# Optimization experiments

Measured on AMD Instinct MI355X. Metric: run time of the kernel, lower is better.

Reference implementation:

```python
import jax, jax.numpy as jnp
import numpy as np

B, C, H, W = 2, 256, 80, 160
G, P, E = 8, 8, 2  # groups(heads), sampling points, ffn expansion
LN_EPS = 1e-5


def setup_inputs() -> dict:
    key = jax.random.key(0)
    ks = jax.random.split(key, 12)
    def n(k, shape, s=1.0):
        return jax.random.normal(k, shape, dtype=jnp.float32) * s
    return dict(
        feats=n(ks[0], (B, C, H, W)),
        feats_pos=n(ks[1], (B, C, H, W)),
        anchor_points=jax.random.uniform(ks[2], (B, H, W, 2), dtype=jnp.float32),
        value_W=n(ks[3], (C, C), 0.02), value_b=jnp.zeros((C,), jnp.float32),
        off_W=n(ks[4], (C, G * P * 2), 0.02), off_b=n(ks[5], (G * P * 2,), 0.02),
        attn_W=n(ks[6], (C, G * P), 0.02), attn_b=jnp.zeros((G * P,), jnp.float32),
        out_W=n(ks[7], (C, C), 0.02), out_b=jnp.zeros((C,), jnp.float32),
        ln1_g=jnp.ones((C,), jnp.float32), ln1_b=jnp.zeros((C,), jnp.float32),
        ln2_g=jnp.ones((C,), jnp.float32), ln2_b=jnp.zeros((C,), jnp.float32),
        ffn_w1=n(ks[8], (E * C, C), 0.02), ffn_b1=jnp.zeros((E * C,), jnp.float32),
        ffn_w2=n(ks[9], (C, E * C), 0.02), ffn_b2=jnp.zeros((C,), jnp.float32),
    )


def _layernorm(x, g, b):
    m = jnp.mean(x, axis=-1, keepdims=True)
    v = jnp.mean(jnp.square(x - m), axis=-1, keepdims=True)
    return (x - m) * jax.lax.rsqrt(v + LN_EPS) * g + b


def _bilinear_sample(value, px, py, h, w):
    # value: [b,G,HW,cg]; px,py: [b,G,P,HW] pixel coords (align_corners=False)
    x0 = jnp.floor(px); y0 = jnp.floor(py)
    wx1 = px - x0; wx0 = 1.0 - wx1
    wy1 = py - y0; wy0 = 1.0 - wy1
    vexp = value[:, :, None, :, :]  # [b,G,1,HW,cg]
    def gather(xi, yi):
        valid = ((xi >= 0) & (xi < w) & (yi >= 0) & (yi < h)).astype(value.dtype)
        xc = jnp.clip(xi, 0, w - 1).astype(jnp.int32)
        yc = jnp.clip(yi, 0, h - 1).astype(jnp.int32)
        idx = yc * w + xc  # [b,G,P,HW]
        v = jnp.take_along_axis(vexp, idx[..., None], axis=3)  # [b,G,P,HW,cg]
        return v * valid[..., None]
    return (gather(x0, y0) * (wx0 * wy0)[..., None]
            + gather(x0 + 1, y0) * (wx1 * wy0)[..., None]
            + gather(x0, y0 + 1) * (wx0 * wy1)[..., None]
            + gather(x0 + 1, y0 + 1) * (wx1 * wy1)[..., None])


def reference(feats, feats_pos, anchor_points,
              value_W, value_b, off_W, off_b, attn_W, attn_b, out_W, out_b,
              ln1_g, ln1_b, ln2_g, ln2_b, ffn_w1, ffn_b1, ffn_w2, ffn_b2):
    b, c, h, w = feats.shape
    hw = h * w
    cg = c // G
    x = feats + feats_pos                              # residual input (pos-encoded)
    q = x.reshape(b, c, hw).transpose(0, 2, 1)         # [b,HW,c]
    # deformable attention
    val = (q @ value_W + value_b).reshape(b, hw, G, cg).transpose(0, 2, 1, 3)   # [b,G,HW,cg]
    off = (q @ off_W + off_b).reshape(b, hw, G, P, 2).transpose(0, 2, 3, 1, 4)  # [b,G,P,HW,2]
    attn = jax.nn.softmax((q @ attn_W + attn_b).reshape(b, hw, G, P)
                          .transpose(0, 2, 3, 1), axis=2)                        # [b,G,P,HW]
    anchor = anchor_points.reshape(b, hw, 2)[:, None, None, :, :]               # [b,1,1,HW,2]
    loc = anchor + off / jnp.array([w, h], dtype=off.dtype)                     # normalized xy
    px = loc[..., 0] * w - 0.5
    py = loc[..., 1] * h - 0.5
    sampled = _bilinear_sample(val, px, py, h, w)                               # [b,G,P,HW,cg]
    agg = jnp.einsum('bgpn,bgpnc->bngc', attn, sampled).reshape(b, hw, c)
    upd = agg @ out_W + out_b
    # residual + LN1
    y = _layernorm(q + upd, ln1_g, ln1_b)
    # conv1x1 - SiLU - conv1x1 FFN + residual + LN2
    ffn = jax.nn.silu(y @ ffn_w1.T + ffn_b1) @ ffn_w2.T + ffn_b2
    y = _layernorm(y + ffn, ln2_g, ln2_b)
    return y.transpose(0, 2, 1).reshape(b, c, h, w)
```

## Files before the change

### kernel.cpp

```cpp
#include <hip/hip_runtime.h>
#include <hip/hip_bf16.h>
#include <math.h>
#include <stdint.h>

#define B_ 2
#define C_ 256
#define H_ 80
#define W_ 160
#define HW_ (H_*W_)
#define NTOK (B_*HW_)
#define G_ 8
#define P_ 8
#define NQKV 448
#define NQKVP 512

typedef __bf16 bf16;
typedef __attribute__((ext_vector_type(8))) __bf16 bf16x8;
typedef __attribute__((ext_vector_type(4))) float f32x4;

__device__ __forceinline__ void gload_lds16(const void* g, void* l) {
  __builtin_amdgcn_global_load_lds(
      (__attribute__((address_space(1))) void*)g,
      (__attribute__((address_space(3))) void*)l,
      16, 0, 0);
}

__global__ __launch_bounds__(256)
void prep_weights(const float* __restrict__ vW, const float* __restrict__ vb,
                  const float* __restrict__ oW, const float* __restrict__ ob,
                  const float* __restrict__ aW, const float* __restrict__ ab,
                  const float* __restrict__ outW,
                  const float* __restrict__ w1, const float* __restrict__ w2,
                  bf16* __restrict__ wqkv, float* __restrict__ bqkv,
                  bf16* __restrict__ woutt, bf16* __restrict__ w1b, bf16* __restrict__ w2b)
{
  int i = blockIdx.x * 256 + threadIdx.x;
  if (i < NQKVP*256) {
    int nn = i >> 8, k = i & 255;
    float w;
    if (nn < 256)      w = vW[k*256 + nn];
    else if (nn < 384) w = oW[k*128 + (nn-256)];
    else if (nn < 448) w = aW[k*64  + (nn-384)];
    else               w = 0.f;
    wqkv[i] = (bf16)w;
  }
  int j = i - NQKVP*256;
  if (j >= 0 && j < 256*256) {
    int nn = j >> 8, k = j & 255;
    woutt[j] = (bf16)outW[k*256 + nn];
  }
  int j2 = i - (NQKVP*256 + 256*256);
  if (j2 >= 0 && j2 < 512*256) w1b[j2] = (bf16)w1[j2];
  int j3 = i - (NQKVP*256 + 256*256 + 512*256);
  if (j3 >= 0 && j3 < 256*512) w2b[j3] = (bf16)w2[j3];
  int j4 = i - (NQKVP*256 + 256*256 + 512*256 + 256*512);
  if (j4 >= 0 && j4 < NQKVP) {
    float bv;
    if (j4 < 256)      bv = vb[j4];
    else if (j4 < 384) bv = ob[j4-256];
    else if (j4 < 448) bv = ab[j4-384];
    else               bv = 0.f;
    bqkv[j4] = bv;
  }
}

__global__ __launch_bounds__(256)
void qprep_kernel(const float* __restrict__ f, const float* __restrict__ fp,
                  bf16* __restrict__ qb)
{
  __shared__ float lt[64][65];
  const int tid = threadIdx.x;
  const int n0 = blockIdx.x * 64;
  const int c0 = blockIdx.y * 64;
  const int b  = blockIdx.z;
#pragma unroll
  for (int i = 0; i < 16; ++i) {
    int cl = i*4 + (tid >> 6), nl = tid & 63;
    size_t gi = ((size_t)(b*C_ + c0 + cl))*HW_ + n0 + nl;
    lt[cl][nl] = f[gi] + fp[gi];
  }
  __syncthreads();
#pragma unroll
  for (int i = 0; i < 16; ++i) {
    int nl = i*4 + (tid >> 6), cl = tid & 63;
    size_t qi = ((size_t)(b*HW_ + n0 + nl))*C_ + c0 + cl;
    qb[qi] = (bf16)lt[cl][nl];
  }
}

template<int EPI, int KTOT>
__global__ __launch_bounds__(256)
void gemm_kernel(const bf16* __restrict__ A, const bf16* __restrict__ Bt,
                 const float* __restrict__ bias,
                 void* __restrict__ out0, float* __restrict__ out1,
                 float* __restrict__ out2, const bf16* __restrict__ resb)
{
  __shared__ bf16 lA[128*64];
  __shared__ bf16 lB[128*64];
  const int tid  = threadIdx.x;
  const int wave = tid >> 6, lane = tid & 63;
  const int m0 = blockIdx.x * 128, n0 = blockIdx.y * 128;
  const int wm = wave >> 1, wn = wave & 1;
  const int fr = lane & 15;
  const int fq = lane >> 4;
  f32x4 acc[4][4] = {};

  for (int kc = 0; kc < KTOT/64; ++kc) {
    if (kc) __syncthreads();
#pragma unroll
    for (int it = 0; it < 4; ++it) {
      int chunk = it*256 + tid;
      int row = chunk >> 3, cb = chunk & 7;
      int ksw = ((cb ^ (row & 7)) << 3);
      gload_lds16(A  + (size_t)(m0+row)*KTOT + kc*64 + ksw,
                  (char*)lA + it*4096 + wave*1024);
      gload_lds16(Bt + (size_t)(n0+row)*KTOT + kc*64 + ksw,
                  (char*)lB + it*4096 + wave*1024);
    }
    __syncthreads();
#pragma unroll
    for (int ks = 0; ks < 2; ++ks) {
      bf16x8 af[4], bg[4];
#pragma unroll
      for (int i = 0; i < 4; ++i) {
        int ar = wm*64 + i*16 + fr;
        af[i] = *(const bf16x8*)&lA[ar*64 + (((ks*4 + fq) ^ (ar & 7)) << 3)];
        int br = wn*64 + i*16 + fr;
        bg[i] = *(const bf16x8*)&lB[br*64 + (((ks*4 + fq) ^ (br & 7)) << 3)];
      }
#pragma unroll
      for (int mi = 0; mi < 4; ++mi)
#pragma unroll
        for (int ni = 0; ni < 4; ++ni)
          acc[mi][ni] = __builtin_amdgcn_mfma_f32_16x16x32_bf16(af[mi], bg[ni], acc[mi][ni], 0, 0, 0);
    }
  }

#pragma unroll
  for (int mi = 0; mi < 4; ++mi)
#pragma unroll
  for (int ni = 0; ni < 4; ++ni)
#pragma unroll
  for (int r = 0; r < 4; ++r) {
    int row = m0 + wm*64 + mi*16 + fq*4 + r;
    int col = n0 + wn*64 + ni*16 + fr;
    float v = acc[mi][ni][r] + bias[col];
    if (EPI == 0) {
      if (col < 256)      ((bf16*)out0)[(size_t)row*256 + col] = (bf16)v;
      else if (col < 384) out1[(size_t)row*128 + (col-256)] = v;
      else if (col < 448) out2[(size_t)row*64  + (col-384)] = v;
    } else if (EPI == 2) {
      float s = v / (1.0f + __expf(-v));
      ((bf16*)out0)[(size_t)row*512 + col] = (bf16)s;
    } else {
      ((float*)out0)[(size_t)row*256 + col] = v + (float)resb[(size_t)row*256 + col];
    }
  }
}

__global__ __launch_bounds__(512)
void gemm_ln_kernel(const bf16* __restrict__ A, const bf16* __restrict__ Bt,
                    const float* __restrict__ bias, const bf16* __restrict__ res,
                    const float* __restrict__ gg, const float* __restrict__ bb,
                    bf16* __restrict__ y1b)
{
  __shared__ bf16 lA[128*64];
  __shared__ bf16 lB[256*64];
  __shared__ float2 red[128][4];
  const int tid  = threadIdx.x;
  const int wave = tid >> 6, lane = tid & 63;
  const int m0 = blockIdx.x * 128;
  const int wm = wave >> 2, wn = wave & 3;
  const int fr = lane & 15;
  const int fq = lane >> 4;
  f32x4 acc[4][4] = {};

  for (int kc = 0; kc < 256/64; ++kc) {
    if (kc) __syncthreads();
#pragma unroll
    for (int it = 0; it < 2; ++it) {
      int chunk = it*512 + tid;
      int row = chunk >> 3, cb = chunk & 7;
      int ksw = ((cb ^ (row & 7)) << 3);
      gload_lds16(A + (size_t)(m0+row)*256 + kc*64 + ksw,
                  (char*)lA + it*8192 + wave*1024);
    }
#pragma unroll
    for (int it = 0; it < 4; ++it) {
      int chunk = it*512 + tid;
      int row = chunk >> 3, cb = chunk & 7;
      int ksw = ((cb ^ (row & 7)) << 3);
      gload_lds16(Bt + (size_t)row*256 + kc*64 + ksw,
                  (char*)lB + it*8192 + wave*1024);
    }
    __syncthreads();
#pragma unroll
    for (int ks = 0; ks < 2; ++ks) {
      bf16x8 af[4], bg[4];
#pragma unroll
      for (int i = 0; i < 4; ++i) {
        int ar = wm*64 + i*16 + fr;
        af[i] = *(const bf16x8*)&lA[ar*64 + (((ks*4 + fq) ^ (ar & 7)) << 3)];
        int br = wn*64 + i*16 + fr;
        bg[i] = *(const bf16x8*)&lB[br*64 + (((ks*4 + fq) ^ (br & 7)) << 3)];
      }
#pragma unroll
      for (int mi = 0; mi < 4; ++mi)
#pragma unroll
        for (int ni = 0; ni < 4; ++ni)
          acc[mi][ni] = __builtin_amdgcn_mfma_f32_16x16x32_bf16(af[mi], bg[ni], acc[mi][ni], 0, 0, 0);
    }
  }

  float gcol[4], bcol[4];
#pragma unroll
  for (int ni = 0; ni < 4; ++ni) {
    int col = wn*64 + ni*16 + fr;
    gcol[ni] = gg[col]; bcol[ni] = bb[col];
  }
#pragma unroll
  for (int mi = 0; mi < 4; ++mi)
#pragma unroll
  for (int r = 0; r < 4; ++r) {
    int rowl = wm*64 + mi*16 + fq*4 + r;
    size_t rowg = (size_t)(m0 + rowl);
    float s = 0.f, q = 0.f;
#pragma unroll
    for (int ni = 0; ni < 4; ++ni) {
      int col = wn*64 + ni*16 + fr;
      float v = acc[mi][ni][r] + bias[col] + (float)res[rowg*256 + col];
      acc[mi][ni][r] = v;
      s += v; q += v*v;
    }
#pragma unroll
    for (int o = 1; o < 16; o <<= 1) { s += __shfl_xor(s, o, 64); q += __shfl_xor(q, o, 64); }
    if (fr == 0) red[rowl][wn] = make_float2(s, q);
  }
  __syncthreads();
#pragma unroll
  for (int mi = 0; mi < 4; ++mi)
#pragma unroll
  for (int r = 0; r < 4; ++r) {
    int rowl = wm*64 + mi*16 + fq*4 + r;
    size_t rowg = (size_t)(m0 + rowl);
    float s = 0.f, q = 0.f;
#pragma unroll
    for (int k = 0; k < 4; ++k) { float2 p = red[rowl][k]; s += p.x; q += p.y; }
    const float mean = s * (1.f/256.f);
    const float var  = q * (1.f/256.f) - mean*mean;
    const float rs   = rsqrtf(var + 1e-5f);
#pragma unroll
    for (int ni = 0; ni < 4; ++ni) {
      int col = wn*64 + ni*16 + fr;
      float y = (acc[mi][ni][r] - mean)*rs*gcol[ni] + bcol[ni];
      y1b[rowg*256 + col] = (bf16)y;
    }
  }
}

__global__ __launch_bounds__(256)
void sample_kernel(const bf16* __restrict__ val, const float* __restrict__ off,
                   const float* __restrict__ attnl, const float* __restrict__ anchors,
                   bf16* __restrict__ agg)
{
  const int tid  = threadIdx.x;
  const int lane = tid & 63;
  const int wv   = tid >> 6;
  const int tsub = lane >> 5;
  const int g    = (lane >> 2) & 7;
  const int c8   = lane & 3;
  const int t    = blockIdx.x * 8 + wv * 2 + tsub;
  const int b    = t / HW_;

  const float2 anc = *(const float2*)(anchors + (size_t)t*2);
  const float ax = anc.x * W_ - 0.5f;
  const float ay = anc.y * H_ - 0.5f;

  const float4 l0 = *(const float4*)(attnl + (size_t)t*64 + g*8);
  const float4 l1 = *(const float4*)(attnl + (size_t)t*64 + g*8 + 4);
  float l[8] = {l0.x, l0.y, l0.z, l0.w, l1.x, l1.y, l1.z, l1.w};
  float mx = l[0];
#pragma unroll
  for (int p = 1; p < 8; ++p) mx = fmaxf(mx, l[p]);
  float s = 0.f;
#pragma unroll
  for (int p = 0; p < 8; ++p) { l[p] = __expf(l[p] - mx); s += l[p]; }
  const float inv = 1.f / s;

  const float4* opv = (const float4*)(off + (size_t)t*128 + g*16);
  const float4 o0 = opv[0], o1 = opv[1], o2 = opv[2], o3 = opv[3];
  const float ox[8] = {o0.x, o0.z, o1.x, o1.z, o2.x, o2.z, o3.x, o3.z};
  const float oy[8] = {o0.y, o0.w, o1.y, o1.w, o2.y, o2.w, o3.y, o3.w};

  const bf16* vb = val + ((size_t)b*HW_)*256 + g*32 + c8*8;

  float a[8] = {};
#pragma unroll
  for (int p = 0; p < 8; ++p) {
    const float px = ax + ox[p], py = ay + oy[p];
    const float x0f = floorf(px), y0f = floorf(py);
    const int x0 = (int)x0f, y0 = (int)y0f;
    const float wx1 = px - x0f, wx0 = 1.f - wx1;
    const float wy1 = py - y0f, wy0 = 1.f - wy1;
    const float ap = l[p] * inv;
    float w00 = ap*wx0*wy0, w10 = ap*wx1*wy0, w01 = ap*wx0*wy1, w11 = ap*wx1*wy1;
    const bool vx0 = (unsigned)x0 < W_, vx1 = (unsigned)(x0+1) < W_;
    const bool vy0 = (unsigned)y0 < H_, vy1 = (unsigned)(y0+1) < H_;
    w00 = (vx0 && vy0) ? w00 : 0.f;  w10 = (vx1 && vy0) ? w10 : 0.f;
    w01 = (vx0 && vy1) ? w01 : 0.f;  w11 = (vx1 && vy1) ? w11 : 0.f;
    const int xc0 = min(max(x0, 0), W_-1),   xc1 = min(max(x0+1, 0), W_-1);
    const int yc0 = min(max(y0, 0), H_-1),   yc1 = min(max(y0+1, 0), H_-1);
    const bf16x8 v00 = *(const bf16x8*)(vb + (size_t)(yc0*W_ + xc0)*256);
    const bf16x8 v10 = *(const bf16x8*)(vb + (size_t)(yc0*W_ + xc1)*256);
    const bf16x8 v01 = *(const bf16x8*)(vb + (size_t)(yc1*W_ + xc0)*256);
    const bf16x8 v11 = *(const bf16x8*)(vb + (size_t)(yc1*W_ + xc1)*256);
#pragma unroll
    for (int c = 0; c < 8; ++c)
      a[c] += w00*(float)v00[c] + w10*(float)v10[c]
            + w01*(float)v01[c] + w11*(float)v11[c];
  }
  bf16 r[8];
#pragma unroll
  for (int c = 0; c < 8; ++c) r[c] = (bf16)a[c];
  *(bf16x8*)(agg + (size_t)t*256 + g*32 + c8*8) = *(bf16x8*)r;
}

__global__ __launch_bounds__(256)
void ln2_out_kernel(const float* __restrict__ x, const float* __restrict__ gg,
                    const float* __restrict__ bb, float* __restrict__ out)
{
  __shared__ float lt[32][257];
  const int tid = threadIdx.x, wave = tid >> 6, lane = tid & 63;
  const int tok0 = blockIdx.x * 32;
#pragma unroll
  for (int t8 = 0; t8 < 8; ++t8) {
    const int tl = wave*8 + t8;
    const size_t tok = tok0 + tl;
    const float4 v = ((const float4*)(x + tok*256))[lane];
    float s = v.x + v.y + v.z + v.w;
    float q = v.x*v.x + v.y*v.y + v.z*v.z + v.w*v.w;
#pragma unroll
    for (int o = 32; o; o >>= 1) { s += __shfl_xor(s, o, 64); q += __shfl_xor(q, o, 64); }
    const float mean = s * (1.f/256.f);
    const float var  = q * (1.f/256.f) - mean*mean;
    const float rs   = rsqrtf(var + 1e-5f);
    const int c = lane*4;
    lt[tl][c+0] = (v.x - mean)*rs*gg[c+0] + bb[c+0];
    lt[tl][c+1] = (v.y - mean)*rs*gg[c+1] + bb[c+1];
    lt[tl][c+2] = (v.z - mean)*rs*gg[c+2] + bb[c+2];
    lt[tl][c+3] = (v.w - mean)*rs*gg[c+3] + bb[c+3];
  }
  __syncthreads();
  const int b  = tok0 / HW_;
  const int n0 = tok0 % HW_;
#pragma unroll
  for (int it = 0; it < 32; ++it) {
    int flat = it*256 + tid;
    int c = flat >> 5, tl = flat & 31;
    out[((size_t)(b*C_ + c))*HW_ + n0 + tl] = lt[tl][c];
  }
}

extern "C" void kernel_launch(void* const* d_in, const int* in_sizes, int n_in,
                              void* d_out, int out_size, void* d_ws, size_t ws_size,
                              hipStream_t stream)
{
  const float* feats   = (const float*)d_in[0];
  const float* featsp  = (const float*)d_in[1];
  const float* anchors = (const float*)d_in[2];
  const float* value_W = (const float*)d_in[3];
  const float* value_b = (const float*)d_in[4];
  const float* off_W   = (const float*)d_in[5];
  const float* off_b   = (const float*)d_in[6];
  const float* attn_W  = (const float*)d_in[7];
  const float* attn_b  = (const float*)d_in[8];
  const float* out_W   = (const float*)d_in[9];
  const float* out_b   = (const float*)d_in[10];
  const float* ln1_g   = (const float*)d_in[11];
  const float* ln1_b   = (const float*)d_in[12];
  const float* ln2_g   = (const float*)d_in[13];
  const float* ln2_b   = (const float*)d_in[14];
  const float* w1      = (const float*)d_in[15];
  const float* b1      = (const float*)d_in[16];
  const float* w2      = (const float*)d_in[17];
  const float* b2      = (const float*)d_in[18];
  float* out = (float*)d_out;

  char* ws = (char*)d_ws;
  size_t cur = 0;
  auto alloc = [&](size_t bytes) -> char* {
    char* p = ws + cur;
    cur += (bytes + 255) & ~(size_t)255;
    return p;
  };
  bf16*  wqkv  = (bf16*) alloc((size_t)NQKVP*256*2);
  bf16*  woutt = (bf16*) alloc((size_t)256*256*2);
  bf16*  w1b   = (bf16*) alloc((size_t)512*256*2);
  bf16*  w2b   = (bf16*) alloc((size_t)256*512*2);
  float* bqkv  = (float*)alloc((size_t)NQKVP*4);
  bf16*  qb    = (bf16*) alloc((size_t)NTOK*256*2);
  bf16*  valb  = (bf16*) alloc((size_t)NTOK*256*2);
  float* offv  = (float*)alloc((size_t)NTOK*128*4);
  float* attnl = (float*)alloc((size_t)NTOK*64*4);
  bf16*  aggb  = (bf16*) alloc((size_t)NTOK*256*2);
  bf16*  y1b   = (bf16*) alloc((size_t)NTOK*256*2);
  bf16*  hb    = (bf16*) alloc((size_t)NTOK*512*2);
  float* x2    = (float*)alloc((size_t)NTOK*256*4);

  prep_weights<<<(NQKVP*256 + 256*256 + 512*256 + 256*512 + NQKVP + 255)/256, 256, 0, stream>>>(
      value_W, value_b, off_W, off_b, attn_W, attn_b, out_W, w1, w2,
      wqkv, bqkv, woutt, w1b, w2b);

  qprep_kernel<<<dim3(HW_/64, C_/64, B_), 256, 0, stream>>>(feats, featsp, qb);

  gemm_kernel<0, 256><<<dim3(NTOK/128, NQKVP/128), 256, 0, stream>>>(
      qb, wqkv, bqkv, valb, offv, attnl, nullptr);

  sample_kernel<<<NTOK/8, 256, 0, stream>>>(valb, offv, attnl, anchors, aggb);

  gemm_ln_kernel<<<NTOK/128, 512, 0, stream>>>(
      aggb, woutt, out_b, qb, ln1_g, ln1_b, y1b);

  gemm_kernel<2, 256><<<dim3(NTOK/128, 512/128), 256, 0, stream>>>(
      y1b, w1b, b1, hb, nullptr, nullptr, nullptr);

  gemm_kernel<3, 512><<<dim3(NTOK/128, 256/128), 256, 0, stream>>>(
      hb, w2b, b2, x2, nullptr, nullptr, y1b);

  ln2_out_kernel<<<NTOK/32, 256, 0, stream>>>(x2, ln2_g, ln2_b, out);
}
```

Measured before the change: 152.9 us.

## Fuse FFN second GEMM with LayerNorm2 and NCHW transpose output

Replaces the FFN down-projection GEMM plus its separate LN2/transpose kernel with the templated gemm_ln_kernel. That kernel now handles KTOT=512, applies LayerNorm in registers, and writes NCHW float output through an LDS transpose that reuses the GEMM shared memory. This removes the fp32 x2 round trip through global memory and one launch. It also swizzles block indices in sample_kernel to spread tokens across blocks, aiming for better cache and channel locality. The fused kernel gains extra syncs and LDS transposes, and the full-row LN forces N=256 per block, which reduces grid parallelism.

```diff
diff --git a/kernel.cpp b/kernel.cpp
--- a/kernel.cpp
+++ b/kernel.cpp
@@ -93,7 +93,7 @@
 void gemm_kernel(const bf16* __restrict__ A, const bf16* __restrict__ Bt,
                  const float* __restrict__ bias,
                  void* __restrict__ out0, float* __restrict__ out1,
-                 float* __restrict__ out2, const bf16* __restrict__ resb)
+                 float* __restrict__ out2)
 {
   __shared__ bf16 lA[128*64];
   __shared__ bf16 lB[128*64];
@@ -149,23 +149,24 @@
       if (col < 256)      ((bf16*)out0)[(size_t)row*256 + col] = (bf16)v;
       else if (col < 384) out1[(size_t)row*128 + (col-256)] = v;
       else if (col < 448) out2[(size_t)row*64  + (col-384)] = v;
-    } else if (EPI == 2) {
+    } else {
       float s = v / (1.0f + __expf(-v));
       ((bf16*)out0)[(size_t)row*512 + col] = (bf16)s;
-    } else {
-      ((float*)out0)[(size_t)row*256 + col] = v + (float)resb[(size_t)row*256 + col];
-    }
-  }
-}
-
+    }
+  }
+}
+
+template<int KTOT, bool NCHW_OUT>
 __global__ __launch_bounds__(512)
 void gemm_ln_kernel(const bf16* __restrict__ A, const bf16* __restrict__ Bt,
                     const float* __restrict__ bias, const bf16* __restrict__ res,
                     const float* __restrict__ gg, const float* __restrict__ bb,
-                    bf16* __restrict__ y1b)
-{
-  __shared__ bf16 lA[128*64];
-  __shared__ bf16 lB[256*64];
+                    bf16* __restrict__ yb, float* __restrict__ outf)
+{
+  __shared__ __align__(16) char smem[49152];
+  bf16* lA = (bf16*)smem;
+  bf16* lB = (bf16*)(smem + 16384);
+  float (*lt)[132] = (float(*)[132])smem;
   __shared__ float2 red[128][4];
   const int tid  = threadIdx.x;
   const int wave = tid >> 6, lane = tid & 63;
@@ -175,14 +176,14 @@
   const int fq = lane >> 4;
   f32x4 acc[4][4] = {};
 
-  for (int kc = 0; kc < 256/64; ++kc) {
+  for (int kc = 0; kc < KTOT/64; ++kc) {
     if (kc) __syncthreads();
 #pragma unroll
     for (int it = 0; it < 2; ++it) {
       int chunk = it*512 + tid;
       int row = chunk >> 3, cb = chunk & 7;
       int ksw = ((cb ^ (row & 7)) << 3);
-      gload_lds16(A + (size_t)(m0+row)*256 + kc*64 + ksw,
+      gload_lds16(A + (size_t)(m0+row)*KTOT + kc*64 + ksw,
                   (char*)lA + it*8192 + wave*1024);
     }
 #pragma unroll
@@ -190,7 +191,7 @@
       int chunk = it*512 + tid;
       int row = chunk >> 3, cb = chunk & 7;
       int ksw = ((cb ^ (row & 7)) << 3);
-      gload_lds16(Bt + (size_t)row*256 + kc*64 + ksw,
+      gload_lds16(Bt + (size_t)row*KTOT + kc*64 + ksw,
                   (char*)lB + it*8192 + wave*1024);
     }
     __syncthreads();
@@ -242,7 +243,6 @@
 #pragma unroll
   for (int r = 0; r < 4; ++r) {
     int rowl = wm*64 + mi*16 + fq*4 + r;
-    size_t rowg = (size_t)(m0 + rowl);
     float s = 0.f, q = 0.f;
 #pragma unroll
     for (int k = 0; k < 4; ++k) { float2 p = red[rowl][k]; s += p.x; q += p.y; }
@@ -250,10 +250,45 @@
     const float var  = q * (1.f/256.f) - mean*mean;
     const float rs   = rsqrtf(var + 1e-5f);
 #pragma unroll
-    for (int ni = 0; ni < 4; ++ni) {
+    for (int ni = 0; ni < 4; ++ni)
+      acc[mi][ni][r] = (acc[mi][ni][r] - mean)*rs*gcol[ni] + bcol[ni];
+  }
+
+  if constexpr (!NCHW_OUT) {
+#pragma unroll
+    for (int mi = 0; mi < 4; ++mi)
+#pragma unroll
+    for (int ni = 0; ni < 4; ++ni)
+#pragma unroll
+    for (int r = 0; r < 4; ++r) {
+      size_t rowg = (size_t)(m0 + wm*64 + mi*16 + fq*4 + r);
       int col = wn*64 + ni*16 + fr;
-      float y = (acc[mi][ni][r] - mean)*rs*gcol[ni] + bcol[ni];
-      y1b[rowg*256 + col] = (bf16)y;
+      yb[rowg*256 + col] = (bf16)acc[mi][ni][r];
+    }
+  } else {
+    const int bq = m0 / HW_;
+    const int n0 = m0 % HW_;
+    __syncthreads();
+#pragma unroll
+    for (int ch = 0; ch < 4; ++ch) {
+      if (ch) __syncthreads();
+      if (wn == ch) {
+#pragma unroll
+        for (int mi = 0; mi < 4; ++mi)
+#pragma unroll
+        for (int ni = 0; ni < 4; ++ni)
+#pragma unroll
+        for (int r = 0; r < 4; ++r)
+          lt[ni*16 + fr][wm*64 + mi*16 + fq*4 + r] = acc[mi][ni][r];
+      }
+      __syncthreads();
+#pragma unroll
+      for (int j = 0; j < 4; ++j) {
+        int flat = j*2048 + tid*4;
+        int cl = flat >> 7, tk = flat & 127;
+        float4 v4 = *(const float4*)&lt[cl][tk];
+        *(float4*)&outf[((size_t)(bq*C_ + ch*64 + cl))*HW_ + n0 + tk] = v4;
+      }
     }
   }
 }
@@ -269,7 +304,9 @@
   const int tsub = lane >> 5;
   const int g    = (lane >> 2) & 7;
   const int c8   = lane & 3;
-  const int t    = blockIdx.x * 8 + wv * 2 + tsub;
+  const int bid  = blockIdx.x;
+  const int swz  = (bid & 7) * ((NTOK/8) >> 3) + (bid >> 3);
+  const int t    = swz * 8 + wv * 2 + tsub;
   const int b    = t / HW_;
 
   const float2 anc = *(const float2*)(anchors + (size_t)t*2);
@@ -323,42 +360,6 @@
 #pragma unroll
   for (int c = 0; c < 8; ++c) r[c] = (bf16)a[c];
   *(bf16x8*)(agg + (size_t)t*256 + g*32 + c8*8) = *(bf16x8*)r;
-}
-
-__global__ __launch_bounds__(256)
-void ln2_out_kernel(const float* __restrict__ x, const float* __restrict__ gg,
-                    const float* __restrict__ bb, float* __restrict__ out)
-{
-  __shared__ float lt[32][257];
-  const int tid = threadIdx.x, wave = tid >> 6, lane = tid & 63;
-  const int tok0 = blockIdx.x * 32;
-#pragma unroll
-  for (int t8 = 0; t8 < 8; ++t8) {
-    const int tl = wave*8 + t8;
-    const size_t tok = tok0 + tl;
-    const float4 v = ((const float4*)(x + tok*256))[lane];
-    float s = v.x + v.y + v.z + v.w;
-    float q = v.x*v.x + v.y*v.y + v.z*v.z + v.w*v.w;
-#pragma unroll
-    for (int o = 32; o; o >>= 1) { s += __shfl_xor(s, o, 64); q += __shfl_xor(q, o, 64); }
-    const float mean = s * (1.f/256.f);
-    const float var  = q * (1.f/256.f) - mean*mean;
-    const float rs   = rsqrtf(var + 1e-5f);
-    const int c = lane*4;
-    lt[tl][c+0] = (v.x - mean)*rs*gg[c+0] + bb[c+0];
-    lt[tl][c+1] = (v.y - mean)*rs*gg[c+1] + bb[c+1];
-    lt[tl][c+2] = (v.z - mean)*rs*gg[c+2] + bb[c+2];
-    lt[tl][c+3] = (v.w - mean)*rs*gg[c+3] + bb[c+3];
-  }
-  __syncthreads();
-  const int b  = tok0 / HW_;
-  const int n0 = tok0 % HW_;
-#pragma unroll
-  for (int it = 0; it < 32; ++it) {
-    int flat = it*256 + tid;
-    int c = flat >> 5, tl = flat & 31;
-    out[((size_t)(b*C_ + c))*HW_ + n0 + tl] = lt[tl][c];
-  }
 }
 
 extern "C" void kernel_launch(void* const* d_in, const int* in_sizes, int n_in,
@@ -405,7 +406,6 @@
   bf16*  aggb  = (bf16*) alloc((size_t)NTOK*256*2);
   bf16*  y1b   = (bf16*) alloc((size_t)NTOK*256*2);
   bf16*  hb    = (bf16*) alloc((size_t)NTOK*512*2);
-  float* x2    = (float*)alloc((size_t)NTOK*256*4);
 
   prep_weights<<<(NQKVP*256 + 256*256 + 512*256 + 256*512 + NQKVP + 255)/256, 256, 0, stream>>>(
       value_W, value_b, off_W, off_b, attn_W, attn_b, out_W, w1, w2,
@@ -414,18 +414,16 @@
   qprep_kernel<<<dim3(HW_/64, C_/64, B_), 256, 0, stream>>>(feats, featsp, qb);
 
   gemm_kernel<0, 256><<<dim3(NTOK/128, NQKVP/128), 256, 0, stream>>>(
-      qb, wqkv, bqkv, valb, offv, attnl, nullptr);
+      qb, wqkv, bqkv, valb, offv, attnl);
 
   sample_kernel<<<NTOK/8, 256, 0, stream>>>(valb, offv, attnl, anchors, aggb);
 
-  gemm_ln_kernel<<<NTOK/128, 512, 0, stream>>>(
-      aggb, woutt, out_b, qb, ln1_g, ln1_b, y1b);
+  gemm_ln_kernel<256, false><<<NTOK/128, 512, 0, stream>>>(
+      aggb, woutt, out_b, qb, ln1_g, ln1_b, y1b, nullptr);
 
   gemm_kernel<2, 256><<<dim3(NTOK/128, 512/128), 256, 0, stream>>>(
-      y1b, w1b, b1, hb, nullptr, nullptr, nullptr);
-
-  gemm_kernel<3, 512><<<dim3(NTOK/128, 256/128), 256, 0, stream>>>(
-      hb, w2b, b2, x2, nullptr, nullptr, y1b);
-
-  ln2_out_kernel<<<NTOK/32, 256, 0, stream>>>(x2, ln2_g, ln2_b, out);
-}
+      y1b, w1b, b1, hb, nullptr, nullptr);
+
+  gemm_ln_kernel<512, true><<<NTOK/128, 512, 0, stream>>>(
+      hb, w2b, b2, y1b, ln2_g, ln2_b, nullptr, out);
+}
```

New measurement: 145.5 us. -4.8%, faster.
